# Performance work log

Measured on AMD Instinct MI355X. Metric: run time of the kernel, lower is better.

Reference implementation:

```python
import jax, jax.numpy as jnp
import numpy as np

HEADS = 4
DIM_HEAD = 64
SCALE = 8.0
EPS = 1e-5  # fp32 branch of the original LayerNorm


def setup_inputs() -> dict:
    key = jax.random.key(0)
    k1, k2, k3 = jax.random.split(key, 3)
    B, C, F, H, W = 2, 256, 4, 32, 32
    inner = HEADS * DIM_HEAD  # 256
    x = jax.random.normal(k1, (B, C, F, H, W), dtype=jnp.float32)
    gamma = jnp.ones((1, C, 1, 1, 1), dtype=jnp.float32)
    w_qkv = jax.random.normal(k2, (3 * inner, C), dtype=jnp.float32) * 0.05
    w_out = jax.random.normal(k3, (C, inner), dtype=jnp.float32) * 0.05
    return {"x": x, "gamma": gamma, "w_qkv": w_qkv, "w_out": w_out}


def _l2norm(t):
    return t / jnp.sqrt(jnp.sum(t * t, axis=-1, keepdims=True) + 1e-12)


def reference(x, gamma, w_qkv, w_out):
    B, C, F, H, W = x.shape
    N = F * H * W
    inner = HEADS * DIM_HEAD
    residual = x

    # channel LayerNorm (biased variance over dim=1)
    mean = jnp.mean(x, axis=1, keepdims=True)
    var = jnp.mean((x - mean) ** 2, axis=1, keepdims=True)
    xn = (x - mean) / jnp.sqrt(var + EPS) * gamma

    # 1x1x1 conv == channel matmul; flatten spatial dims to sequence
    xn_flat = xn.reshape(B, C, N)                      # [B, C, N]
    qkv = jnp.einsum('oc,bcn->bon', w_qkv, xn_flat)    # [B, 3*inner, N]
    qkv = qkv.reshape(B, 3, HEADS, DIM_HEAD, N)        # chunk then split heads
    qkv = jnp.transpose(qkv, (1, 0, 2, 4, 3))          # [3, B, h, N, d]
    q, k, v = qkv[0], qkv[1], qkv[2]

    q = _l2norm(q)
    k = _l2norm(k)

    sim = jnp.einsum('bhid,bhjd->bhij', q, k) * SCALE  # [B, h, N, N]
    attn = jax.nn.softmax(sim, axis=-1)
    out = jnp.einsum('bhij,bhjd->bhid', attn, v)       # [B, h, N, d]

    # 'b h n d -> b (h d) n' then 1x1x1 out conv
    out = jnp.transpose(out, (0, 1, 3, 2)).reshape(B, inner, N)
    out = jnp.einsum('oi,bin->bon', w_out, out).reshape(B, C, F, H, W)
    return out + residual
```

## Files before the change

kernel.cpp:

```cpp
#include <hip/hip_runtime.h>

#define BATCH 2
#define CCH   256
#define NSEQ  4096
#define NH    4
#define DH    64
#define INNER 256

typedef __attribute__((ext_vector_type(8))) __bf16 bf16x8;
typedef __attribute__((ext_vector_type(4))) float f32x4;
typedef __attribute__((ext_vector_type(8))) unsigned short u16x8;
typedef __attribute__((ext_vector_type(4))) unsigned short u16x4;

#define GLD16(gsrc, ldst)                                                     \
  __builtin_amdgcn_global_load_lds(                                           \
      (const __attribute__((address_space(1))) unsigned int*)(const void*)(gsrc), \
      (__attribute__((address_space(3))) unsigned int*)(void*)(ldst), 16, 0, 0)

static __device__ __forceinline__ unsigned short f2bfr(float f) {
  union { float f; unsigned u; } v; v.f = f;
  return (unsigned short)((v.u + 0x8000u) >> 16);
}
static __device__ __forceinline__ unsigned pack2(float f0, float f1) {
  union { float f; unsigned u; } a, b; a.f = f0; b.f = f1;
  return __builtin_amdgcn_perm(b.u + 0x8000u, a.u + 0x8000u, 0x07060302u);
}
static __device__ __forceinline__ unsigned cvtpk(float lo, float hi) {
  unsigned r;
  asm("v_cvt_pk_bf16_f32 %0, %1, %2" : "=v"(r) : "v"(lo), "v"(hi));
  return r;
}
static __device__ __forceinline__ float bf2f(unsigned short u) {
  union { unsigned u; float f; } v; v.u = ((unsigned)u) << 16;
  return v.f;
}
static __device__ __forceinline__ bf16x8 ldb(const unsigned short* p) {
  return *(const bf16x8*)p;
}
static __device__ __forceinline__ f32x4 mm(bf16x8 a, bf16x8 b, f32x4 c) {
  return __builtin_amdgcn_mfma_f32_16x16x32_bf16(a, b, c, 0, 0, 0);
}
static __device__ __forceinline__ float ex2(float x) {
  return __builtin_amdgcn_exp2f(x);
}

__global__ __launch_bounds__(256) void k_lncvt(const float* __restrict__ x,
                                               const float* __restrict__ gamma,
                                               unsigned short* __restrict__ xn,
                                               const float* __restrict__ wq,
                                               const float* __restrict__ wo,
                                               unsigned short* __restrict__ wqb,
                                               unsigned short* __restrict__ wob) {
  int blk = blockIdx.x;
  if (blk >= 256) {
    int t = (blk - 256) * 256 + threadIdx.x;
    int e = t * 4;
    if (e < 768 * 256) {
      float4 v = *(const float4*)(wq + e);
      u16x4 pk = { f2bfr(v.x), f2bfr(v.y), f2bfr(v.z), f2bfr(v.w) };
      *(u16x4*)(wqb + e) = pk;
    } else {
      int e2 = e - 768 * 256;
      float4 v = *(const float4*)(wo + e2);
      u16x4 pk = { f2bfr(v.x), f2bfr(v.y), f2bfr(v.z), f2bfr(v.w) };
      *(u16x4*)(wob + e2) = pk;
    }
    return;
  }
  int b  = blk >> 7;
  int n0 = (blk & 127) * 32;
  int t  = threadIdx.x;
  int nl = t & 31;
  int cg = t >> 5;
  int n  = n0 + nl;
  const float* xp = x + ((size_t)(b * CCH + cg * 32)) * NSEQ + n;
  float vals[32];
  float s = 0.f, s2 = 0.f;
#pragma unroll
  for (int j = 0; j < 32; j++) {
    float v = xp[(size_t)j * NSEQ];
    vals[j] = v; s += v; s2 += v * v;
  }
  __shared__ float rs[8][32], rs2[8][32];
  rs[cg][nl] = s; rs2[cg][nl] = s2;
  __syncthreads();
  float S = 0.f, S2 = 0.f;
#pragma unroll
  for (int g = 0; g < 8; g++) { S += rs[g][nl]; S2 += rs2[g][nl]; }
  float mean = S * (1.f / 256.f);
  float var  = S2 * (1.f / 256.f) - mean * mean;
  float rstd = rsqrtf(var + 1e-5f);
  unsigned short* dst = xn + ((size_t)b * NSEQ + n) * CCH + cg * 32;
#pragma unroll
  for (int j0 = 0; j0 < 32; j0 += 8) {
    u16x8 pk;
#pragma unroll
    for (int j = 0; j < 8; j++)
      pk[j] = f2bfr((vals[j0 + j] - mean) * rstd * gamma[cg * 32 + j0 + j]);
    *(u16x8*)(dst + j0) = pk;
  }
}

__global__ __launch_bounds__(256) void k_qkv(const unsigned short* __restrict__ wqb,
                                             const unsigned short* __restrict__ xn,
                                             unsigned short* __restrict__ qkv,
                                             unsigned short* __restrict__ qt,
                                             unsigned short* __restrict__ ktb) {
  int n0 = blockIdx.x * 64;
  int oi = blockIdx.y;
  int o0 = oi * 64;
  int b  = blockIdx.z;
  __shared__ unsigned short Al[64 * 128];
  __shared__ unsigned short Bl[64 * 128];
  int t = threadIdx.x;
  int lane = t & 63, w = t >> 6;
  int c = lane & 15, quad = lane >> 4;
  int wm = w >> 1, wn = w & 1;
  f32x4 acc[2][2] = {};
  int lr = lane >> 4;
  int lchk = lane & 15;
  const unsigned short* apg = wqb + (size_t)o0 * CCH;
  const unsigned short* bpg = xn + ((size_t)b * NSEQ + n0) * CCH;
  for (int kt = 0; kt < 2; kt++) {
    if (kt) __syncthreads();
#pragma unroll
    for (int q = 0; q < 4; q++) {
      int r = w * 16 + q * 4 + lr;
      int srcoff = r * CCH + kt * 128 + ((lchk ^ (r & 7)) * 8);
      GLD16(apg + srcoff, Al + (size_t)(w * 16 + q * 4) * 128);
      GLD16(bpg + srcoff, Bl + (size_t)(w * 16 + q * 4) * 128);
    }
    __syncthreads();
#pragma unroll
    for (int ks = 0; ks < 4; ks++) {
      int ra0 = wm * 32 + c, ra1 = ra0 + 16;
      int rb0 = wn * 32 + c, rb1 = rb0 + 16;
      bf16x8 a0 = ldb(&Al[ra0 * 128 + (((ks * 4 + quad) ^ (ra0 & 7)) * 8)]);
      bf16x8 a1 = ldb(&Al[ra1 * 128 + (((ks * 4 + quad) ^ (ra1 & 7)) * 8)]);
      bf16x8 b0 = ldb(&Bl[rb0 * 128 + (((ks * 4 + quad) ^ (rb0 & 7)) * 8)]);
      bf16x8 b1 = ldb(&Bl[rb1 * 128 + (((ks * 4 + quad) ^ (rb1 & 7)) * 8)]);
      acc[0][0] = mm(a0, b0, acc[0][0]);
      acc[0][1] = mm(a0, b1, acc[0][1]);
      acc[1][0] = mm(a1, b0, acc[1][0]);
      acc[1][1] = mm(a1, b1, acc[1][1]);
    }
  }
  if (oi < 8) {
    float* sq = (float*)Al;
    float s0 = 0.f, s1 = 0.f;
#pragma unroll
    for (int i = 0; i < 2; i++)
#pragma unroll
      for (int rr = 0; rr < 4; rr++) {
        s0 += acc[i][0][rr] * acc[i][0][rr];
        s1 += acc[i][1][rr] * acc[i][1][rr];
      }
    s0 += __shfl_xor(s0, 16); s0 += __shfl_xor(s0, 32);
    s1 += __shfl_xor(s1, 16); s1 += __shfl_xor(s1, 32);
    __syncthreads();
    if (quad == 0) {
      sq[wm * 64 + wn * 32 + c]      = s0;
      sq[wm * 64 + wn * 32 + 16 + c] = s1;
    }
    __syncthreads();
    float r0 = rsqrtf(sq[wn * 32 + c]      + sq[64 + wn * 32 + c]      + 1e-12f);
    float r1 = rsqrtf(sq[wn * 32 + 16 + c] + sq[64 + wn * 32 + 16 + c] + 1e-12f);
    if (oi < 4) { r0 *= 11.541560327111707f; r1 *= 11.541560327111707f; }
    int h = oi & 3;
    unsigned short* base = (oi < 4 ? qt : ktb) + ((size_t)(b * NH + h) * NSEQ) * DH;
#pragma unroll
    for (int i = 0; i < 2; i++)
#pragma unroll
      for (int j = 0; j < 2; j++) {
        float rsc = j ? r1 : r0;
        int n = n0 + wn * 32 + j * 16 + c;
        int d = wm * 32 + i * 16 + quad * 4;
        uint2 pk = { pack2(acc[i][j][0] * rsc, acc[i][j][1] * rsc),
                     pack2(acc[i][j][2] * rsc, acc[i][j][3] * rsc) };
        *(uint2*)(base + (size_t)n * DH + d) = pk;
      }
  } else {
#pragma unroll
    for (int i = 0; i < 2; i++)
#pragma unroll
      for (int j = 0; j < 2; j++)
#pragma unroll
        for (int rr = 0; rr < 4; rr++) {
          int o = o0 + wm * 32 + i * 16 + quad * 4 + rr;
          int n = n0 + wn * 32 + j * 16 + c;
          qkv[((size_t)b * 768 + o) * NSEQ + n] = f2bfr(acc[i][j][rr]);
        }
  }
}

__global__ __launch_bounds__(256, 2) void k_attn(
    const unsigned short* __restrict__ qt,
    const unsigned short* __restrict__ ktb,
    const unsigned short* __restrict__ qkv,
    unsigned short* __restrict__ opart,
    float* __restrict__ lpart,
    int S, int kvlen) {
  int i0 = blockIdx.x * 256;
  int h  = blockIdx.y;
  int bz = blockIdx.z;
  int b  = bz / S, s = bz % S;
  __shared__ unsigned short Kl[2][64 * 64];
  __shared__ unsigned short Vl[2][64 * 64];
  int t = threadIdx.x;
  int lane = t & 63, w = t >> 6;
  int c = lane & 15, quad = lane >> 4;

  const unsigned short* qbase = qt  + ((size_t)(b * NH + h) * NSEQ) * DH;
  const unsigned short* kbase = ktb + ((size_t)(b * NH + h) * NSEQ) * DH;
  const unsigned short* vbase = qkv + ((size_t)b * 768 + 512 + h * 64) * NSEQ;

  bf16x8 qa[4], qb[4];
#pragma unroll
  for (int ss = 0; ss < 4; ss++) {
    const unsigned short* qp =
        qbase + (size_t)(i0 + w * 64 + ss * 16 + c) * DH + quad * 8;
    qa[ss] = ldb(qp); qb[ss] = ldb(qp + 32);
  }

  u16x8 onesu;
#pragma unroll
  for (int j = 0; j < 8; j++) onesu[j] = 0x3F80;
  bf16x8 ones = *(bf16x8*)&onesu;

  f32x4 acc[4][4] = {};
  f32x4 accl[4]  = {};

  int slr = lane >> 3, slc = lane & 7;
  int ssw_v  = (slc ^ slr) * 8;
  int ssw_k1 = (slc ^ (slr & 3)) * 8;
  int ssw_k2 = ssw_k1 ^ 32;
  const unsigned short* kp = kbase + (size_t)(s * kvlen + w * 16 + slr) * DH;
  const unsigned short* vp = vbase + (size_t)(w * 16 + slr) * NSEQ + s * kvlen + ssw_v;
  int sw0 = (quad ^ (c & 7)) * 8;
  int sw1 = sw0 ^ 32;
  int fK    = (c & 3) | (((c >> 2) & 1) << 2);
  int swk0  = (quad ^ fK) * 8;
  int swk1  = swk0 ^ 32;
  int krow0 = (c >> 2) * 8 + (c & 3);

  int nIt = kvlen / 64;
  GLD16(kp + ssw_k1,          &Kl[0][(w * 16)     * 64]);
  GLD16(kp + 8 * DH + ssw_k2, &Kl[0][(w * 16 + 8) * 64]);
  GLD16(vp,                   &Vl[0][(w * 16)     * 64]);
  GLD16(vp + 8 * NSEQ,        &Vl[0][(w * 16 + 8) * 64]);
  kp += 64 * DH; vp += 64;

  union U4 { unsigned u[4]; bf16x8 v; };
  U4 p0[4], p1[4];

#define QKSET(qA, qB, P0, P1)                                                 \
  {                                                                           \
    f32x4 z0 = {}, z1 = {}, z2 = {}, z3 = {};                                 \
    __builtin_amdgcn_s_setprio(1);                                            \
    z0 = mm(k00, qA, z0); z0 = mm(k01, qB, z0);                               \
    z1 = mm(k10, qA, z1); z1 = mm(k11, qB, z1);                               \
    z2 = mm(k20, qA, z2); z2 = mm(k21, qB, z2);                               \
    z3 = mm(k30, qA, z3); z3 = mm(k31, qB, z3);                               \
    __builtin_amdgcn_s_setprio(0);                                            \
    P0.u[0] = cvtpk(ex2(z0[0]), ex2(z0[1]));                                  \
    P0.u[1] = cvtpk(ex2(z0[2]), ex2(z0[3]));                                  \
    P0.u[2] = cvtpk(ex2(z1[0]), ex2(z1[1]));                                  \
    P0.u[3] = cvtpk(ex2(z1[2]), ex2(z1[3]));                                  \
    P1.u[0] = cvtpk(ex2(z2[0]), ex2(z2[1]));                                  \
    P1.u[1] = cvtpk(ex2(z2[2]), ex2(z2[3]));                                  \
    P1.u[2] = cvtpk(ex2(z3[0]), ex2(z3[1]));                                  \
    P1.u[3] = cvtpk(ex2(z3[2]), ex2(z3[3]));                                  \
  }

  for (int it = 0; it < nIt; it++) {
    int cur = it & 1;
    __syncthreads();
    if (it + 1 < nIt) {
      int nb = cur ^ 1;
      GLD16(kp + ssw_k1,          &Kl[nb][(w * 16)     * 64]);
      GLD16(kp + 8 * DH + ssw_k2, &Kl[nb][(w * 16 + 8) * 64]);
      GLD16(vp,                   &Vl[nb][(w * 16)     * 64]);
      GLD16(vp + 8 * NSEQ,        &Vl[nb][(w * 16 + 8) * 64]);
      kp += 64 * DH; vp += 64;
    }

    const unsigned short* Kb = &Kl[cur][0];
    bf16x8 k00 = ldb(&Kb[(krow0)      * 64 + swk0]);
    bf16x8 k01 = ldb(&Kb[(krow0)      * 64 + swk1]);
    bf16x8 k10 = ldb(&Kb[(krow0 + 4)  * 64 + swk0]);
    bf16x8 k11 = ldb(&Kb[(krow0 + 4)  * 64 + swk1]);
    bf16x8 k20 = ldb(&Kb[(krow0 + 32) * 64 + swk0]);
    bf16x8 k21 = ldb(&Kb[(krow0 + 32) * 64 + swk1]);
    bf16x8 k30 = ldb(&Kb[(krow0 + 36) * 64 + swk0]);
    bf16x8 k31 = ldb(&Kb[(krow0 + 36) * 64 + swk1]);

    QKSET(qa[0], qb[0], p0[0], p1[0]);
    QKSET(qa[1], qb[1], p0[1], p1[1]);
    QKSET(qa[2], qb[2], p0[2], p1[2]);
    QKSET(qa[3], qb[3], p0[3], p1[3]);

#pragma unroll
    for (int dt = 0; dt < 4; dt++) {
      bf16x8 v0 = ldb(&Vl[cur][(dt * 16 + c) * 64 + sw0]);
      bf16x8 v1 = ldb(&Vl[cur][(dt * 16 + c) * 64 + sw1]);
      __builtin_amdgcn_s_setprio(1);
#pragma unroll
      for (int ss = 0; ss < 4; ss++) {
        acc[ss][dt] = mm(p0[ss].v, v0, acc[ss][dt]);
        acc[ss][dt] = mm(p1[ss].v, v1, acc[ss][dt]);
      }
      __builtin_amdgcn_s_setprio(0);
    }
    __builtin_amdgcn_s_setprio(1);
#pragma unroll
    for (int ss = 0; ss < 4; ss++) {
      accl[ss] = mm(p0[ss].v, ones, accl[ss]);
      accl[ss] = mm(p1[ss].v, ones, accl[ss]);
    }
    __builtin_amdgcn_s_setprio(0);
  }
#undef QKSET

  size_t rb = ((size_t)(b * NH + h) * S + s) * NSEQ + i0 + w * 64;
#pragma unroll
  for (int ss = 0; ss < 4; ss++) {
    size_t rbs = rb + ss * 16;
    if (c == 0) {
#pragma unroll
      for (int rr = 0; rr < 4; rr++)
        lpart[rbs + quad * 4 + rr] = accl[ss][rr];
    }
#pragma unroll
    for (int rr = 0; rr < 4; rr++)
#pragma unroll
      for (int dt = 0; dt < 4; dt++)
        opart[(rbs + quad * 4 + rr) * 64 + dt * 16 + c] = f2bfr(acc[ss][dt][rr]);
  }
}

__global__ __launch_bounds__(256) void k_merge(
    const unsigned short* __restrict__ opart,
    const float* __restrict__ lpart,
    unsigned short* __restrict__ ao, int S) {
  int t = blockIdx.x * 256 + threadIdx.x;
  int row = t >> 2;
  int dseg = (t & 3) * 16;
  int b = row >> 14, rem = row & 16383;
  int h = rem >> 12, i = rem & 4095;

  float l = 0.f;
  float o[16];
#pragma unroll
  for (int j = 0; j < 16; j++) o[j] = 0.f;
  for (int s = 0; s < S; s++) {
    size_t rb = ((size_t)(b * NH + h) * S + s) * NSEQ + i;
    l += lpart[rb];
    const unsigned short* p = opart + rb * 64 + dseg;
    u16x8 v0 = *(const u16x8*)p;
    u16x8 v1 = *(const u16x8*)(p + 8);
#pragma unroll
    for (int j = 0; j < 8; j++) {
      o[j]     += bf2f(v0[j]);
      o[8 + j] += bf2f(v1[j]);
    }
  }
  float inv = 1.f / l;
  unsigned short* dst = ao + ((size_t)b * NSEQ + i) * INNER + h * 64 + dseg;
  uint4 pk0 = { pack2(o[0] * inv, o[1] * inv),  pack2(o[2] * inv, o[3] * inv),
                pack2(o[4] * inv, o[5] * inv),  pack2(o[6] * inv, o[7] * inv) };
  uint4 pk1 = { pack2(o[8] * inv, o[9] * inv),  pack2(o[10] * inv, o[11] * inv),
                pack2(o[12] * inv, o[13] * inv),pack2(o[14] * inv, o[15] * inv) };
  *(uint4*)dst = pk0;
  *(uint4*)(dst + 8) = pk1;
}

__global__ __launch_bounds__(256) void k_out(const unsigned short* __restrict__ wob,
                                             const unsigned short* __restrict__ ao,
                                             const float* __restrict__ x,
                                             float* __restrict__ out) {
  int n0 = blockIdx.x * 64;
  int o0 = blockIdx.y * 64;
  int b  = blockIdx.z;
  __shared__ unsigned short Al[64 * 128];
  __shared__ unsigned short Bl[64 * 128];
  int t = threadIdx.x;
  int lane = t & 63, w = t >> 6;
  int c = lane & 15, quad = lane >> 4;
  int wm = w >> 1, wn = w & 1;
  f32x4 acc[2][2] = {};
  int lr = lane >> 4;
  int lchk = lane & 15;
  const unsigned short* apg = wob + (size_t)o0 * INNER;
  const unsigned short* bpg = ao + ((size_t)b * NSEQ + n0) * INNER;
  for (int kt = 0; kt < 2; kt++) {
    if (kt) __syncthreads();
#pragma unroll
    for (int q = 0; q < 4; q++) {
      int r = w * 16 + q * 4 + lr;
      int srcoff = r * INNER + kt * 128 + ((lchk ^ (r & 7)) * 8);
      GLD16(apg + srcoff, Al + (size_t)(w * 16 + q * 4) * 128);
      GLD16(bpg + srcoff, Bl + (size_t)(w * 16 + q * 4) * 128);
    }
    __syncthreads();
#pragma unroll
    for (int ks = 0; ks < 4; ks++) {
      int ra0 = wm * 32 + c, ra1 = ra0 + 16;
      int rb0 = wn * 32 + c, rb1 = rb0 + 16;
      bf16x8 a0 = ldb(&Al[ra0 * 128 + (((ks * 4 + quad) ^ (ra0 & 7)) * 8)]);
      bf16x8 a1 = ldb(&Al[ra1 * 128 + (((ks * 4 + quad) ^ (ra1 & 7)) * 8)]);
      bf16x8 b0 = ldb(&Bl[rb0 * 128 + (((ks * 4 + quad) ^ (rb0 & 7)) * 8)]);
      bf16x8 b1 = ldb(&Bl[rb1 * 128 + (((ks * 4 + quad) ^ (rb1 & 7)) * 8)]);
      acc[0][0] = mm(a0, b0, acc[0][0]);
      acc[0][1] = mm(a0, b1, acc[0][1]);
      acc[1][0] = mm(a1, b0, acc[1][0]);
      acc[1][1] = mm(a1, b1, acc[1][1]);
    }
  }
#pragma unroll
  for (int i = 0; i < 2; i++)
#pragma unroll
    for (int j = 0; j < 2; j++)
#pragma unroll
      for (int rr = 0; rr < 4; rr++) {
        int o = o0 + wm * 32 + i * 16 + quad * 4 + rr;
        int n = n0 + wn * 32 + j * 16 + c;
        size_t idx = ((size_t)b * CCH + o) * NSEQ + n;
        out[idx] = acc[i][j][rr] + x[idx];
      }
}

extern "C" void kernel_launch(void* const* d_in, const int* in_sizes, int n_in,
                              void* d_out, int out_size, void* d_ws, size_t ws_size,
                              hipStream_t stream) {
  const float* x     = (const float*)d_in[0];
  const float* gamma = (const float*)d_in[1];
  const float* wq    = (const float*)d_in[2];
  const float* wo    = (const float*)d_in[3];
  float* out = (float*)d_out;

  const size_t MB = 1u << 20;
  char* ws = (char*)d_ws;
  unsigned short* ao  = (unsigned short*)ws;
  unsigned short* xn  = (unsigned short*)(ws + 4 * MB);
  unsigned short* qkv = (unsigned short*)(ws + 8 * MB);
  unsigned short* wqb = (unsigned short*)(ws + 20 * MB);
  unsigned short* wob = (unsigned short*)(ws + 20 * MB + 512 * 1024);
  unsigned short* qt  = (unsigned short*)(ws + 21 * MB);
  unsigned short* ktb = (unsigned short*)(ws + 25 * MB);
  unsigned short* opart = (unsigned short*)(ws + 29 * MB);
  int S;
  if (ws_size >= 48 * MB) S = 4;
  else if (ws_size >= 40 * MB) S = 2;
  else S = 1;
  size_t opart_bytes = (size_t)S * BATCH * NH * NSEQ * DH * 2;
  float* lpart = (float*)(ws + 29 * MB + opart_bytes);
  int kvlen = NSEQ / S;

  k_lncvt<<<dim3(512),          256, 0, stream>>>(x, gamma, xn, wq, wo, wqb, wob);
  k_qkv  <<<dim3(64, 12, 2),    256, 0, stream>>>(wqb, xn, qkv, qt, ktb);
  k_attn <<<dim3(16, 4, 2 * S), 256, 0, stream>>>(qt, ktb, qkv, opart,
                                                  lpart, S, kvlen);
  k_merge<<<dim3(512),          256, 0, stream>>>(opart, lpart, ao, S);
  k_out  <<<dim3(64, 4, 2),     256, 0, stream>>>(wob, ao, x, out);
}
```

Baseline: 124.0 us.

## Software-pipeline QK and PV in attention and fuse split-merge into out projection

The attention loop is restructured so the QK^T exponentials for tile it are computed while the PV MMAs for tile it-1 run, using two ping-pong P register sets. V loads are delayed one stage behind K, and a final PV drain follows the loop. Separately, the k_merge kernel is removed: k_out now reduces the split-K partial outputs and normalizes by l directly into shared memory before the output GEMM. This drops one launch and the ao round trip, but k_out redoes the merge four times (once per output-channel block) and the P registers double, which raises register pressure.

```diff
diff --git a/kernel.cpp b/kernel.cpp
--- a/kernel.cpp
+++ b/kernel.cpp
@@ -246,12 +246,10 @@
   int nIt = kvlen / 64;
   GLD16(kp + ssw_k1,          &Kl[0][(w * 16)     * 64]);
   GLD16(kp + 8 * DH + ssw_k2, &Kl[0][(w * 16 + 8) * 64]);
-  GLD16(vp,                   &Vl[0][(w * 16)     * 64]);
-  GLD16(vp + 8 * NSEQ,        &Vl[0][(w * 16 + 8) * 64]);
-  kp += 64 * DH; vp += 64;
+  kp += 64 * DH;
 
   union U4 { unsigned u[4]; bf16x8 v; };
-  U4 p0[4], p1[4];
+  U4 pA0[4], pA1[4], pB0[4], pB1[4];
 
 #define QKSET(qA, qB, P0, P1)                                                 \
   {                                                                           \
@@ -272,53 +270,83 @@
     P1.u[3] = cvtpk(ex2(z3[2]), ex2(z3[3]));                                  \
   }
 
-  for (int it = 0; it < nIt; it++) {
-    int cur = it & 1;
-    __syncthreads();
-    if (it + 1 < nIt) {
-      int nb = cur ^ 1;
-      GLD16(kp + ssw_k1,          &Kl[nb][(w * 16)     * 64]);
-      GLD16(kp + 8 * DH + ssw_k2, &Kl[nb][(w * 16 + 8) * 64]);
-      GLD16(vp,                   &Vl[nb][(w * 16)     * 64]);
-      GLD16(vp + 8 * NSEQ,        &Vl[nb][(w * 16 + 8) * 64]);
-      kp += 64 * DH; vp += 64;
-    }
-
-    const unsigned short* Kb = &Kl[cur][0];
-    bf16x8 k00 = ldb(&Kb[(krow0)      * 64 + swk0]);
-    bf16x8 k01 = ldb(&Kb[(krow0)      * 64 + swk1]);
-    bf16x8 k10 = ldb(&Kb[(krow0 + 4)  * 64 + swk0]);
-    bf16x8 k11 = ldb(&Kb[(krow0 + 4)  * 64 + swk1]);
-    bf16x8 k20 = ldb(&Kb[(krow0 + 32) * 64 + swk0]);
-    bf16x8 k21 = ldb(&Kb[(krow0 + 32) * 64 + swk1]);
-    bf16x8 k30 = ldb(&Kb[(krow0 + 36) * 64 + swk0]);
-    bf16x8 k31 = ldb(&Kb[(krow0 + 36) * 64 + swk1]);
-
-    QKSET(qa[0], qb[0], p0[0], p1[0]);
-    QKSET(qa[1], qb[1], p0[1], p1[1]);
-    QKSET(qa[2], qb[2], p0[2], p1[2]);
-    QKSET(qa[3], qb[3], p0[3], p1[3]);
-
-#pragma unroll
-    for (int dt = 0; dt < 4; dt++) {
-      bf16x8 v0 = ldb(&Vl[cur][(dt * 16 + c) * 64 + sw0]);
-      bf16x8 v1 = ldb(&Vl[cur][(dt * 16 + c) * 64 + sw1]);
-      __builtin_amdgcn_s_setprio(1);
-#pragma unroll
-      for (int ss = 0; ss < 4; ss++) {
-        acc[ss][dt] = mm(p0[ss].v, v0, acc[ss][dt]);
-        acc[ss][dt] = mm(p1[ss].v, v1, acc[ss][dt]);
-      }
-      __builtin_amdgcn_s_setprio(0);
-    }
-    __builtin_amdgcn_s_setprio(1);
-#pragma unroll
-    for (int ss = 0; ss < 4; ss++) {
-      accl[ss] = mm(p0[ss].v, ones, accl[ss]);
-      accl[ss] = mm(p1[ss].v, ones, accl[ss]);
-    }
-    __builtin_amdgcn_s_setprio(0);
-  }
+#define PVD(dt, Vb, PO0, PO1)                                                 \
+  {                                                                           \
+    bf16x8 v0 = ldb(&Vb[((dt) * 16 + c) * 64 + sw0]);                         \
+    bf16x8 v1 = ldb(&Vb[((dt) * 16 + c) * 64 + sw1]);                         \
+    __builtin_amdgcn_s_setprio(1);                                            \
+    acc[0][dt] = mm(PO0[0].v, v0, acc[0][dt]);                                \
+    acc[0][dt] = mm(PO1[0].v, v1, acc[0][dt]);                                \
+    acc[1][dt] = mm(PO0[1].v, v0, acc[1][dt]);                                \
+    acc[1][dt] = mm(PO1[1].v, v1, acc[1][dt]);                                \
+    acc[2][dt] = mm(PO0[2].v, v0, acc[2][dt]);                                \
+    acc[2][dt] = mm(PO1[2].v, v1, acc[2][dt]);                                \
+    acc[3][dt] = mm(PO0[3].v, v0, acc[3][dt]);                                \
+    acc[3][dt] = mm(PO1[3].v, v1, acc[3][dt]);                                \
+    __builtin_amdgcn_s_setprio(0);                                            \
+  }
+
+#define ACCL(PO0, PO1)                                                        \
+  __builtin_amdgcn_s_setprio(1);                                              \
+  accl[0] = mm(PO0[0].v, ones, accl[0]); accl[0] = mm(PO1[0].v, ones, accl[0]); \
+  accl[1] = mm(PO0[1].v, ones, accl[1]); accl[1] = mm(PO1[1].v, ones, accl[1]); \
+  accl[2] = mm(PO0[2].v, ones, accl[2]); accl[2] = mm(PO1[2].v, ones, accl[2]); \
+  accl[3] = mm(PO0[3].v, ones, accl[3]); accl[3] = mm(PO1[3].v, ones, accl[3]); \
+  __builtin_amdgcn_s_setprio(0);
+
+#define ITER(IT, PN0, PN1, PO0, PO1, DO_PV)                                   \
+  {                                                                           \
+    __syncthreads();    \
+    if ((IT) + 1 < nIt) {                                                     \
+      unsigned short* kd = &Kl[((IT) + 1) & 1][0];                            \
+      GLD16(kp + ssw_k1,          kd + (w * 16) * 64);                        \
+      GLD16(kp + 8 * DH + ssw_k2, kd + (w * 16 + 8) * 64);                    \
+      kp += 64 * DH;                                                          \
+    }                                                                         \
+    {                                                                         \
+      unsigned short* vd = &Vl[(IT) & 1][0];                                  \
+      GLD16(vp,            vd + (w * 16) * 64);                               \
+      GLD16(vp + 8 * NSEQ, vd + (w * 16 + 8) * 64);                           \
+      vp += 64;                                                               \
+    }                                                                         \
+    const unsigned short* Kb = &Kl[(IT) & 1][0];                              \
+    const unsigned short* Vb = &Vl[((IT) + 1) & 1][0];       \
+    bf16x8 k00 = ldb(&Kb[(krow0)      * 64 + swk0]);                          \
+    bf16x8 k01 = ldb(&Kb[(krow0)      * 64 + swk1]);                          \
+    bf16x8 k10 = ldb(&Kb[(krow0 + 4)  * 64 + swk0]);                          \
+    bf16x8 k11 = ldb(&Kb[(krow0 + 4)  * 64 + swk1]);                          \
+    bf16x8 k20 = ldb(&Kb[(krow0 + 32) * 64 + swk0]);                          \
+    bf16x8 k21 = ldb(&Kb[(krow0 + 32) * 64 + swk1]);                          \
+    bf16x8 k30 = ldb(&Kb[(krow0 + 36) * 64 + swk0]);                          \
+    bf16x8 k31 = ldb(&Kb[(krow0 + 36) * 64 + swk1]);                          \
+    QKSET(qa[0], qb[0], PN0[0], PN1[0]);                                      \
+    if (DO_PV) PVD(0, Vb, PO0, PO1);                                          \
+    QKSET(qa[1], qb[1], PN0[1], PN1[1]);                                      \
+    if (DO_PV) PVD(1, Vb, PO0, PO1);                                          \
+    QKSET(qa[2], qb[2], PN0[2], PN1[2]);                                      \
+    if (DO_PV) PVD(2, Vb, PO0, PO1);                                          \
+    QKSET(qa[3], qb[3], PN0[3], PN1[3]);                                      \
+    if (DO_PV) PVD(3, Vb, PO0, PO1);                                          \
+    if (DO_PV) { ACCL(PO0, PO1); }                                            \
+  }
+
+  for (int itp = 0; itp < nIt / 2; ++itp) {
+    int it0 = itp * 2;
+    ITER(it0,     pA0, pA1, pB0, pB1, (itp > 0));
+    ITER(it0 + 1, pB0, pB1, pA0, pA1, 1);
+  }
+  __syncthreads();
+  {
+    const unsigned short* Vb = &Vl[1][0];
+    PVD(0, Vb, pB0, pB1);
+    PVD(1, Vb, pB0, pB1);
+    PVD(2, Vb, pB0, pB1);
+    PVD(3, Vb, pB0, pB1);
+    ACCL(pB0, pB1);
+  }
+#undef ITER
+#undef ACCL
+#undef PVD
 #undef QKSET
 
   size_t rb = ((size_t)(b * NH + h) * S + s) * NSEQ + i0 + w * 64;
@@ -338,83 +366,71 @@
   }
 }
 
-__global__ __launch_bounds__(256) void k_merge(
-    const unsigned short* __restrict__ opart,
-    const float* __restrict__ lpart,
-    unsigned short* __restrict__ ao, int S) {
-  int t = blockIdx.x * 256 + threadIdx.x;
-  int row = t >> 2;
-  int dseg = (t & 3) * 16;
-  int b = row >> 14, rem = row & 16383;
-  int h = rem >> 12, i = rem & 4095;
-
-  float l = 0.f;
-  float o[16];
-#pragma unroll
-  for (int j = 0; j < 16; j++) o[j] = 0.f;
-  for (int s = 0; s < S; s++) {
-    size_t rb = ((size_t)(b * NH + h) * S + s) * NSEQ + i;
-    l += lpart[rb];
-    const unsigned short* p = opart + rb * 64 + dseg;
-    u16x8 v0 = *(const u16x8*)p;
-    u16x8 v1 = *(const u16x8*)(p + 8);
-#pragma unroll
-    for (int j = 0; j < 8; j++) {
-      o[j]     += bf2f(v0[j]);
-      o[8 + j] += bf2f(v1[j]);
-    }
-  }
-  float inv = 1.f / l;
-  unsigned short* dst = ao + ((size_t)b * NSEQ + i) * INNER + h * 64 + dseg;
-  uint4 pk0 = { pack2(o[0] * inv, o[1] * inv),  pack2(o[2] * inv, o[3] * inv),
-                pack2(o[4] * inv, o[5] * inv),  pack2(o[6] * inv, o[7] * inv) };
-  uint4 pk1 = { pack2(o[8] * inv, o[9] * inv),  pack2(o[10] * inv, o[11] * inv),
-                pack2(o[12] * inv, o[13] * inv),pack2(o[14] * inv, o[15] * inv) };
-  *(uint4*)dst = pk0;
-  *(uint4*)(dst + 8) = pk1;
-}
-
 __global__ __launch_bounds__(256) void k_out(const unsigned short* __restrict__ wob,
-                                             const unsigned short* __restrict__ ao,
+                                             const unsigned short* __restrict__ opart,
+                                             const float* __restrict__ lpart,
                                              const float* __restrict__ x,
-                                             float* __restrict__ out) {
+                                             float* __restrict__ out, int S) {
   int n0 = blockIdx.x * 64;
   int o0 = blockIdx.y * 64;
   int b  = blockIdx.z;
-  __shared__ unsigned short Al[64 * 128];
-  __shared__ unsigned short Bl[64 * 128];
+  __shared__ unsigned short Al[64 * 256];
+  __shared__ unsigned short Bl[64 * 256];
   int t = threadIdx.x;
   int lane = t & 63, w = t >> 6;
   int c = lane & 15, quad = lane >> 4;
   int wm = w >> 1, wn = w & 1;
+  int lr2 = lane >> 5, lch = lane & 31;
+  const unsigned short* apg = wob + (size_t)o0 * INNER;
+#pragma unroll
+  for (int q = 0; q < 8; q++) {
+    int r = w * 16 + q * 2 + lr2;
+    int srcoff = r * INNER + ((lch ^ (r & 7)) * 8);
+    GLD16(apg + srcoff, Al + (size_t)(w * 16 + q * 2) * 256);
+  }
+  int n_l = t >> 2;
+  int seg = t & 3;
+#pragma unroll
+  for (int hh = 0; hh < 4; hh++) {
+    float l = 0.f;
+    float o[16];
+#pragma unroll
+    for (int j = 0; j < 16; j++) o[j] = 0.f;
+    for (int s = 0; s < S; s++) {
+      size_t rbm = ((size_t)(b * NH + hh) * S + s) * NSEQ + n0 + n_l;
+      l += lpart[rbm];
+      const unsigned short* p = opart + rbm * 64 + seg * 16;
+      u16x8 v0 = *(const u16x8*)p;
+      u16x8 v1 = *(const u16x8*)(p + 8);
+#pragma unroll
+      for (int j = 0; j < 8; j++) {
+        o[j]     += bf2f(v0[j]);
+        o[8 + j] += bf2f(v1[j]);
+      }
+    }
+    float inv = 1.f / l;
+    int cc = hh * 8 + seg * 2;
+    uint4 pkA = { pack2(o[0] * inv,  o[1] * inv),  pack2(o[2] * inv,  o[3] * inv),
+                  pack2(o[4] * inv,  o[5] * inv),  pack2(o[6] * inv,  o[7] * inv) };
+    uint4 pkB = { pack2(o[8] * inv,  o[9] * inv),  pack2(o[10] * inv, o[11] * inv),
+                  pack2(o[12] * inv, o[13] * inv), pack2(o[14] * inv, o[15] * inv) };
+    *(uint4*)&Bl[n_l * 256 + (((cc)     ^ (n_l & 7)) * 8)] = pkA;
+    *(uint4*)&Bl[n_l * 256 + (((cc + 1) ^ (n_l & 7)) * 8)] = pkB;
+  }
+  __syncthreads();
   f32x4 acc[2][2] = {};
-  int lr = lane >> 4;
-  int lchk = lane & 15;
-  const unsigned short* apg = wob + (size_t)o0 * INNER;
-  const unsigned short* bpg = ao + ((size_t)b * NSEQ + n0) * INNER;
-  for (int kt = 0; kt < 2; kt++) {
-    if (kt) __syncthreads();
-#pragma unroll
-    for (int q = 0; q < 4; q++) {
-      int r = w * 16 + q * 4 + lr;
-      int srcoff = r * INNER + kt * 128 + ((lchk ^ (r & 7)) * 8);
-      GLD16(apg + srcoff, Al + (size_t)(w * 16 + q * 4) * 128);
-      GLD16(bpg + srcoff, Bl + (size_t)(w * 16 + q * 4) * 128);
-    }
-    __syncthreads();
-#pragma unroll
-    for (int ks = 0; ks < 4; ks++) {
-      int ra0 = wm * 32 + c, ra1 = ra0 + 16;
-      int rb0 = wn * 32 + c, rb1 = rb0 + 16;
-      bf16x8 a0 = ldb(&Al[ra0 * 128 + (((ks * 4 + quad) ^ (ra0 & 7)) * 8)]);
-      bf16x8 a1 = ldb(&Al[ra1 * 128 + (((ks * 4 + quad) ^ (ra1 & 7)) * 8)]);
-      bf16x8 b0 = ldb(&Bl[rb0 * 128 + (((ks * 4 + quad) ^ (rb0 & 7)) * 8)]);
-      bf16x8 b1 = ldb(&Bl[rb1 * 128 + (((ks * 4 + quad) ^ (rb1 & 7)) * 8)]);
-      acc[0][0] = mm(a0, b0, acc[0][0]);
-      acc[0][1] = mm(a0, b1, acc[0][1]);
-      acc[1][0] = mm(a1, b0, acc[1][0]);
-      acc[1][1] = mm(a1, b1, acc[1][1]);
-    }
+#pragma unroll
+  for (int ks = 0; ks < 8; ks++) {
+    int ra0 = wm * 32 + c, ra1 = ra0 + 16;
+    int rb0 = wn * 32 + c, rb1 = rb0 + 16;
+    bf16x8 a0 = ldb(&Al[ra0 * 256 + (((ks * 4 + quad) ^ (ra0 & 7)) * 8)]);
+    bf16x8 a1 = ldb(&Al[ra1 * 256 + (((ks * 4 + quad) ^ (ra1 & 7)) * 8)]);
+    bf16x8 b0 = ldb(&Bl[rb0 * 256 + (((ks * 4 + quad) ^ (rb0 & 7)) * 8)]);
+    bf16x8 b1 = ldb(&Bl[rb1 * 256 + (((ks * 4 + quad) ^ (rb1 & 7)) * 8)]);
+    acc[0][0] = mm(a0, b0, acc[0][0]);
+    acc[0][1] = mm(a0, b1, acc[0][1]);
+    acc[1][0] = mm(a1, b0, acc[1][0]);
+    acc[1][1] = mm(a1, b1, acc[1][1]);
   }
 #pragma unroll
   for (int i = 0; i < 2; i++)
@@ -440,7 +456,6 @@
 
   const size_t MB = 1u << 20;
   char* ws = (char*)d_ws;
-  unsigned short* ao  = (unsigned short*)ws;
   unsigned short* xn  = (unsigned short*)(ws + 4 * MB);
   unsigned short* qkv = (unsigned short*)(ws + 8 * MB);
   unsigned short* wqb = (unsigned short*)(ws + 20 * MB);
@@ -460,6 +475,5 @@
   k_qkv  <<<dim3(64, 12, 2),    256, 0, stream>>>(wqb, xn, qkv, qt, ktb);
   k_attn <<<dim3(16, 4, 2 * S), 256, 0, stream>>>(qt, ktb, qkv, opart,
                                                   lpart, S, kvlen);
-  k_merge<<<dim3(512),          256, 0, stream>>>(opart, lpart, ao, S);
-  k_out  <<<dim3(64, 4, 2),     256, 0, stream>>>(wob, ao, x, out);
-}
+  k_out  <<<dim3(64, 4, 2),     256, 0, stream>>>(wob, opart, lpart, x, out, S);
+}
```

Result: slower. 128.1 us (+3.3%).

## Fuse split-KV merge into attention kernel via last-block atomic counter

Applied to the files above, without the earlier changes.

Removes the separate merge kernel launch. Each attention block now bumps a per-tile atomic counter, and the last of the S split blocks for a tile reduces the partial outputs and denominators and writes the normalized result. The counters are zeroed in the first kernel. This saves one launch and its tail, but the reduction is serialized onto a subset of blocks and adds thread fences and atomics.

```diff
diff --git a/kernel.cpp b/kernel.cpp
--- a/kernel.cpp
+++ b/kernel.cpp
@@ -50,9 +50,11 @@
                                                const float* __restrict__ wq,
                                                const float* __restrict__ wo,
                                                unsigned short* __restrict__ wqb,
-                                               unsigned short* __restrict__ wob) {
+                                               unsigned short* __restrict__ wob,
+                                               int* __restrict__ cnt) {
   int blk = blockIdx.x;
   if (blk >= 256) {
+    if (blk == 256 && threadIdx.x < 128) cnt[threadIdx.x] = 0;
     int t = (blk - 256) * 256 + threadIdx.x;
     int e = t * 4;
     if (e < 768 * 256) {
@@ -199,6 +201,8 @@
     const unsigned short* __restrict__ qkv,
     unsigned short* __restrict__ opart,
     float* __restrict__ lpart,
+    unsigned short* __restrict__ ao,
+    int* __restrict__ cnt,
     int S, int kvlen) {
   int i0 = blockIdx.x * 256;
   int h  = blockIdx.y;
@@ -336,42 +340,51 @@
       for (int dt = 0; dt < 4; dt++)
         opart[(rbs + quad * 4 + rr) * 64 + dt * 16 + c] = f2bfr(acc[ss][dt][rr]);
   }
-}
-
-__global__ __launch_bounds__(256) void k_merge(
-    const unsigned short* __restrict__ opart,
-    const float* __restrict__ lpart,
-    unsigned short* __restrict__ ao, int S) {
-  int t = blockIdx.x * 256 + threadIdx.x;
-  int row = t >> 2;
-  int dseg = (t & 3) * 16;
-  int b = row >> 14, rem = row & 16383;
-  int h = rem >> 12, i = rem & 4095;
-
-  float l = 0.f;
-  float o[16];
-#pragma unroll
-  for (int j = 0; j < 16; j++) o[j] = 0.f;
-  for (int s = 0; s < S; s++) {
-    size_t rb = ((size_t)(b * NH + h) * S + s) * NSEQ + i;
-    l += lpart[rb];
-    const unsigned short* p = opart + rb * 64 + dseg;
-    u16x8 v0 = *(const u16x8*)p;
-    u16x8 v1 = *(const u16x8*)(p + 8);
-#pragma unroll
-    for (int j = 0; j < 8; j++) {
-      o[j]     += bf2f(v0[j]);
-      o[8 + j] += bf2f(v1[j]);
-    }
-  }
-  float inv = 1.f / l;
-  unsigned short* dst = ao + ((size_t)b * NSEQ + i) * INNER + h * 64 + dseg;
-  uint4 pk0 = { pack2(o[0] * inv, o[1] * inv),  pack2(o[2] * inv, o[3] * inv),
-                pack2(o[4] * inv, o[5] * inv),  pack2(o[6] * inv, o[7] * inv) };
-  uint4 pk1 = { pack2(o[8] * inv, o[9] * inv),  pack2(o[10] * inv, o[11] * inv),
-                pack2(o[12] * inv, o[13] * inv),pack2(o[14] * inv, o[15] * inv) };
-  *(uint4*)dst = pk0;
-  *(uint4*)(dst + 8) = pk1;
+
+  __threadfence();
+  __shared__ int lastFlag;
+  __syncthreads();
+  if (t == 0) {
+    int idx = ((b * NH + h) << 4) + (i0 >> 8);
+    lastFlag = (atomicAdd(&cnt[idx], 1) == S - 1);
+  }
+  __syncthreads();
+  if (lastFlag) {
+    __threadfence();
+    int n = i0 + t;
+    size_t rbase = ((size_t)(b * NH + h) * S) * NSEQ + n;
+    float l = 0.f;
+    for (int s2 = 0; s2 < S; s2++) l += lpart[rbase + (size_t)s2 * NSEQ];
+    float inv = 1.f / l;
+    unsigned short* dst = ao + ((size_t)b * NSEQ + n) * INNER + h * 64;
+#pragma unroll
+    for (int dc = 0; dc < 4; dc++) {
+      float o[16];
+#pragma unroll
+      for (int j = 0; j < 16; j++) o[j] = 0.f;
+      for (int s2 = 0; s2 < S; s2++) {
+        const unsigned short* p =
+            opart + (rbase + (size_t)s2 * NSEQ) * 64 + dc * 16;
+        u16x8 v0 = *(const u16x8*)p;
+        u16x8 v1 = *(const u16x8*)(p + 8);
+#pragma unroll
+        for (int j = 0; j < 8; j++) {
+          o[j]     += bf2f(v0[j]);
+          o[8 + j] += bf2f(v1[j]);
+        }
+      }
+      uint4 pk0 = { pack2(o[0] * inv,  o[1] * inv),
+                    pack2(o[2] * inv,  o[3] * inv),
+                    pack2(o[4] * inv,  o[5] * inv),
+                    pack2(o[6] * inv,  o[7] * inv) };
+      uint4 pk1 = { pack2(o[8] * inv,  o[9] * inv),
+                    pack2(o[10] * inv, o[11] * inv),
+                    pack2(o[12] * inv, o[13] * inv),
+                    pack2(o[14] * inv, o[15] * inv) };
+      *(uint4*)(dst + dc * 16)     = pk0;
+      *(uint4*)(dst + dc * 16 + 8) = pk1;
+    }
+  }
 }
 
 __global__ __launch_bounds__(256) void k_out(const unsigned short* __restrict__ wob,
@@ -445,6 +458,7 @@
   unsigned short* qkv = (unsigned short*)(ws + 8 * MB);
   unsigned short* wqb = (unsigned short*)(ws + 20 * MB);
   unsigned short* wob = (unsigned short*)(ws + 20 * MB + 512 * 1024);
+  int* cnt            = (int*)(ws + 20 * MB + 768 * 1024);
   unsigned short* qt  = (unsigned short*)(ws + 21 * MB);
   unsigned short* ktb = (unsigned short*)(ws + 25 * MB);
   unsigned short* opart = (unsigned short*)(ws + 29 * MB);
@@ -456,10 +470,9 @@
   float* lpart = (float*)(ws + 29 * MB + opart_bytes);
   int kvlen = NSEQ / S;
 
-  k_lncvt<<<dim3(512),          256, 0, stream>>>(x, gamma, xn, wq, wo, wqb, wob);
+  k_lncvt<<<dim3(512),          256, 0, stream>>>(x, gamma, xn, wq, wo, wqb, wob, cnt);
   k_qkv  <<<dim3(64, 12, 2),    256, 0, stream>>>(wqb, xn, qkv, qt, ktb);
   k_attn <<<dim3(16, 4, 2 * S), 256, 0, stream>>>(qt, ktb, qkv, opart,
-                                                  lpart, S, kvlen);
-  k_merge<<<dim3(512),          256, 0, stream>>>(opart, lpart, ao, S);
+                                                  lpart, ao, cnt, S, kvlen);
   k_out  <<<dim3(64, 4, 2),     256, 0, stream>>>(wob, ao, x, out);
 }
```

Measured after the change: 211.0 us. +70.1%, slower.
